# Kernel tuning notes

Measured on AMD Instinct MI355X. Metric: run time of the kernel, lower is better.

## Reference

```python
import jax, jax.numpy as jnp
import numpy as np

NEG_BIG = -9e15  # matches torch's -9000000000000000.0 mask value
ALPHA = 0.2      # LeakyReLU negative slope


def setup_inputs() -> dict:
    key = jax.random.key(0)
    k1, k2, k3 = jax.random.split(key, 3)
    B, N, Fin, Fout = 8, 2048, 64, 64
    h = jax.random.normal(k1, (B, N, Fin), dtype=jnp.float32)
    adj = jax.random.randint(k2, (B, N, N), 0, 2, dtype=jnp.int32)
    kW, ka = jax.random.split(k3)
    # xavier_uniform with gain=1.414
    gW = 1.414 * np.sqrt(6.0 / (Fin + Fout))
    W = jax.random.uniform(kW, (Fin, Fout), minval=-gW, maxval=gW, dtype=jnp.float32)
    ga = 1.414 * np.sqrt(6.0 / (2 * Fout + 1))
    a = jax.random.uniform(ka, (2 * Fout, 1), minval=-ga, maxval=ga, dtype=jnp.float32)
    return {"h": h, "adj": adj, "W": W, "a": a}


def reference(h, adj, W, a):
    # Wh: [B, N, Fout]
    Wh = jnp.einsum("bnf,fo->bno", h, W)
    Fout = W.shape[1]
    a1 = a[:Fout, 0]   # source part of attention vector
    a2 = a[Fout:, 0]   # target part
    # e_ij = leakyrelu(a1.Wh_i + a2.Wh_j) -- rank-1 decomposition of the
    # repeat/cat construction; avoids the [B,N,N,2F] intermediate.
    s = Wh @ a1        # [B, N]
    t = Wh @ a2        # [B, N]
    e = s[:, :, None] + t[:, None, :]            # [B, N, N]
    e = jnp.where(e > 0, e, ALPHA * e)           # LeakyReLU
    e = jnp.where(adj > 0, e, NEG_BIG)           # adjacency mask
    attention = jax.nn.softmax(e, axis=2)
    # dropout omitted: reference is eval-mode (F.dropout is identity when not training)
    h_prime = jnp.einsum("bij,bjo->bio", attention, Wh)
    return jax.nn.elu(h_prime)                   # concat=True branch
```

## Files before the change

kernel.cpp:

```cpp
#include <hip/hip_runtime.h>


#define ALPHA 0.2f

typedef __attribute__((ext_vector_type(8))) short  short8;
typedef __attribute__((ext_vector_type(4))) float  f32x4;

static __device__ __forceinline__ unsigned short f2bf(float f) {
    unsigned u = __builtin_bit_cast(unsigned, f);
    u += 0x7fffu + ((u >> 16) & 1u);
    return (unsigned short)(u >> 16);
}

static __device__ __forceinline__ unsigned pack_bf2(float lo, float hi) {
    unsigned ulo = __builtin_bit_cast(unsigned, lo) + 0x8000u;
    unsigned uhi = __builtin_bit_cast(unsigned, hi) + 0x8000u;
    return __builtin_amdgcn_perm(uhi, ulo, 0x07060302);
}

__global__ __launch_bounds__(256) void k01(
    const float* __restrict__ h, const int* __restrict__ adj,
    const float* __restrict__ W, const float* __restrict__ a,
    uint4* __restrict__ whF, float* __restrict__ sw,
    float* __restrict__ tw, unsigned char* __restrict__ mask)
{
    __shared__ float W_l[64 * 65];
    __shared__ float wa[128];
    __shared__ float tile[4 * 16 * 65];

    const int tid = threadIdx.x;

    if (blockIdx.x >= 256) {
        const int mb = blockIdx.x - 256;
        const int4* a4 = (const int4*)adj;
        #pragma unroll 1
        for (int g0 = 0; g0 < 16; g0 += 4) {
            int4 v0a, v0b, v1a, v1b, v2a, v2b, v3a, v3b;
            const size_t p0 = (size_t)mb * 4096 + (size_t)g0 * 256 + tid;
            v0a = a4[p0 * 2];          v0b = a4[p0 * 2 + 1];
            v1a = a4[(p0 + 256) * 2];  v1b = a4[(p0 + 256) * 2 + 1];
            v2a = a4[(p0 + 512) * 2];  v2b = a4[(p0 + 512) * 2 + 1];
            v3a = a4[(p0 + 768) * 2];  v3b = a4[(p0 + 768) * 2 + 1];
            unsigned b0 = (v0a.x ? 1u:0u)|(v0a.y ? 2u:0u)|(v0a.z ? 4u:0u)|(v0a.w ? 8u:0u)
                        | (v0b.x ?16u:0u)|(v0b.y ?32u:0u)|(v0b.z ?64u:0u)|(v0b.w ?128u:0u);
            unsigned b1 = (v1a.x ? 1u:0u)|(v1a.y ? 2u:0u)|(v1a.z ? 4u:0u)|(v1a.w ? 8u:0u)
                        | (v1b.x ?16u:0u)|(v1b.y ?32u:0u)|(v1b.z ?64u:0u)|(v1b.w ?128u:0u);
            unsigned b2 = (v2a.x ? 1u:0u)|(v2a.y ? 2u:0u)|(v2a.z ? 4u:0u)|(v2a.w ? 8u:0u)
                        | (v2b.x ?16u:0u)|(v2b.y ?32u:0u)|(v2b.z ?64u:0u)|(v2b.w ?128u:0u);
            unsigned b3 = (v3a.x ? 1u:0u)|(v3a.y ? 2u:0u)|(v3a.z ? 4u:0u)|(v3a.w ? 8u:0u)
                        | (v3b.x ?16u:0u)|(v3b.y ?32u:0u)|(v3b.z ?64u:0u)|(v3b.w ?128u:0u);
            mask[p0]       = (unsigned char)b0;
            mask[p0 + 256] = (unsigned char)b1;
            mask[p0 + 512] = (unsigned char)b2;
            mask[p0 + 768] = (unsigned char)b3;
        }
        return;
    }

    const int lane = tid & 63, wv = tid >> 6;
    const int im   = lane & 15, kq = lane >> 4;

    #pragma unroll
    for (int k = 0; k < 16; ++k) {
        int e = tid + 256 * k;
        W_l[(e >> 6) * 65 + (e & 63)] = W[e];
    }
    __syncthreads();

    if (tid < 128) {
        int f = tid & 63;
        const float* ap = a + (tid >> 6) * 64;
        float acc = 0.f;
        #pragma unroll 8
        for (int o = 0; o < 64; ++o) acc += W_l[f * 65 + o] * ap[o];
        wa[tid] = acc;
    }
    __syncthreads();

    short8 bf[4][2];
    #pragma unroll
    for (int nb = 0; nb < 4; ++nb)
        #pragma unroll
        for (int ks = 0; ks < 2; ++ks)
            #pragma unroll
            for (int u = 0; u < 8; ++u)
                bf[nb][ks][u] = (short)f2bf(W_l[(ks * 32 + kq * 8 + u) * 65 + nb * 16 + im]);

    const int row0 = blockIdx.x * 64 + wv * 16;
    const float* hrow = h + (size_t)(row0 + im) * 64;

    float hv[2][8];
    short8 af[2];
    float sp = 0.f, tp = 0.f;
    #pragma unroll
    for (int ks = 0; ks < 2; ++ks) {
        float4 A = *(const float4*)(hrow + ks * 32 + kq * 8);
        float4 Bv = *(const float4*)(hrow + ks * 32 + kq * 8 + 4);
        hv[ks][0] = A.x;  hv[ks][1] = A.y;  hv[ks][2] = A.z;  hv[ks][3] = A.w;
        hv[ks][4] = Bv.x; hv[ks][5] = Bv.y; hv[ks][6] = Bv.z; hv[ks][7] = Bv.w;
        #pragma unroll
        for (int u = 0; u < 8; ++u) {
            int f = ks * 32 + kq * 8 + u;
            sp += hv[ks][u] * wa[f];
            tp += hv[ks][u] * wa[64 + f];
            af[ks][u] = (short)f2bf(hv[ks][u]);
        }
    }
    sp += __shfl_xor(sp, 16, 64); sp += __shfl_xor(sp, 32, 64);
    tp += __shfl_xor(tp, 16, 64); tp += __shfl_xor(tp, 32, 64);
    if (lane < 16) {
        sw[row0 + lane] = sp;
        tw[row0 + lane] = tp;
    }

    f32x4 acc[4] = {{0.f,0.f,0.f,0.f},{0.f,0.f,0.f,0.f},{0.f,0.f,0.f,0.f},{0.f,0.f,0.f,0.f}};
    #pragma unroll
    for (int ks = 0; ks < 2; ++ks)
        #pragma unroll
        for (int nb = 0; nb < 4; ++nb)
            acc[nb] = __builtin_amdgcn_mfma_f32_16x16x32_bf16(af[ks], bf[nb][ks], acc[nb], 0, 0, 0);

    #pragma unroll
    for (int nb = 0; nb < 4; ++nb)
        #pragma unroll
        for (int r = 0; r < 4; ++r)
            tile[wv * 1040 + (kq * 4 + r) * 65 + nb * 16 + im] = acc[nb][r];
    __syncthreads();

    {
        const int blk_row0 = blockIdx.x * 64;
        const int bb2 = blk_row0 >> 11;
        const int c_base = (blk_row0 & 2047) >> 5;
        #pragma unroll
        for (int k = 0; k < 2; ++k) {
            int e = tid + 256 * k;
            int l = e & 63, ot = (e >> 6) & 3, cl_ = e >> 8;
            int o = ot * 16 + (l & 15);
            int jb = cl_ * 32 + (l >> 4) * 8;
            unsigned d0, d1, d2, d3;
            {
                int j0 = jb;
                d0 = pack_bf2(tile[(j0 >> 4) * 1040 + (j0 & 15) * 65 + o],
                              tile[(j0 >> 4) * 1040 + ((j0 & 15) + 1) * 65 + o]);
                j0 = jb + 2;
                d1 = pack_bf2(tile[(j0 >> 4) * 1040 + (j0 & 15) * 65 + o],
                              tile[(j0 >> 4) * 1040 + ((j0 & 15) + 1) * 65 + o]);
                j0 = jb + 4;
                d2 = pack_bf2(tile[(j0 >> 4) * 1040 + (j0 & 15) * 65 + o],
                              tile[(j0 >> 4) * 1040 + ((j0 & 15) + 1) * 65 + o]);
                j0 = jb + 6;
                d3 = pack_bf2(tile[(j0 >> 4) * 1040 + (j0 & 15) * 65 + o],
                              tile[(j0 >> 4) * 1040 + ((j0 & 15) + 1) * 65 + o]);
            }
            uint4 val = {d0, d1, d2, d3};
            whF[(size_t)(((bb2 * 64 + c_base + cl_) * 4 + ot)) * 64 + l] = val;
        }
    }
}

__global__ __launch_bounds__(256, 2) void k2_attn(
    const unsigned* __restrict__ mask, const uint4* __restrict__ whF,
    const float* __restrict__ sw, const float* __restrict__ tw,
    float* __restrict__ out)
{
    __shared__ float eB[2048];
    __shared__ float eD[2048];
    __shared__ float cpart[4 * 1040];
    __shared__ float zp[64];

    const int tid  = threadIdx.x;
    const int lane = tid & 63, wv = tid >> 6;
    const int im   = lane & 15, kq = lane >> 4;
    const int b    = blockIdx.x >> 7;
    const int i0   = (blockIdx.x & 127) << 4;

    {
        const float4* tp4 = (const float4*)(tw + (size_t)b * 2048);
        float4 t0 = tp4[tid], t1 = tp4[tid + 256];
        float4 e0 = {__expf(t0.x), __expf(t0.y), __expf(t0.z), __expf(t0.w)};
        float4 e1 = {__expf(t1.x), __expf(t1.y), __expf(t1.z), __expf(t1.w)};
        float4 f0 = {__expf(ALPHA*t0.x), __expf(ALPHA*t0.y), __expf(ALPHA*t0.z), __expf(ALPHA*t0.w)};
        float4 f1 = {__expf(ALPHA*t1.x), __expf(ALPHA*t1.y), __expf(ALPHA*t1.z), __expf(ALPHA*t1.w)};
        *(float4*)&eB[tid * 4] = e0;  *(float4*)&eB[(tid + 256) * 4] = e1;
        *(float4*)&eD[tid * 4] = f0;  *(float4*)&eD[(tid + 256) * 4] = f1;
    }

    const uint4* mrow4 = (const uint4*)(mask + (size_t)(b * 2048 + i0 + im) * 64 + wv * 16);
    const uint4 mA = mrow4[0], mB = mrow4[1], mC = mrow4[2], mD = mrow4[3];
    const unsigned mm[16] = {mA.x, mA.y, mA.z, mA.w, mB.x, mB.y, mB.z, mB.w,
                             mC.x, mC.y, mC.z, mC.w, mD.x, mD.y, mD.z, mD.w};

    const float sl = sw[b * 2048 + i0 + im];
    const float al = __expf(sl), cl_ = __expf(ALPHA * sl);
    const int j00 = wv * 512 + kq * 8;
    const uint4* wbase = whF + (size_t)((b * 64 + wv * 16) * 4) * 64 + lane;

    __syncthreads();

    f32x4 acc0 = {0.f,0.f,0.f,0.f}, acc1 = {0.f,0.f,0.f,0.f};
    f32x4 acc2 = {0.f,0.f,0.f,0.f}, acc3 = {0.f,0.f,0.f,0.f};
    float zs = 0.f;

    #pragma unroll
    for (int s = 0; s < 16; ++s) {
        const uint4 w0 = wbase[(s * 4 + 0) * 64];
        const uint4 w1 = wbase[(s * 4 + 1) * 64];
        const uint4 w2 = wbase[(s * 4 + 2) * 64];
        const uint4 w3 = wbase[(s * 4 + 3) * 64];

        const float4 bA = *(const float4*)&eB[j00 + s * 32];
        const float4 bBv = *(const float4*)&eB[j00 + s * 32 + 4];
        const float4 dA = *(const float4*)&eD[j00 + s * 32];
        const float4 dBv = *(const float4*)&eD[j00 + s * 32 + 4];
        const unsigned mbyte = (mm[s] >> (kq * 8)) & 0xffu;

        float m0 = al * bA.x, n0 = cl_ * dA.x;
        float m1 = al * bA.y, n1 = cl_ * dA.y;
        float m2 = al * bA.z, n2 = cl_ * dA.z;
        float m3 = al * bA.w, n3 = cl_ * dA.w;
        float m4 = al * bBv.x, n4 = cl_ * dBv.x;
        float m5 = al * bBv.y, n5 = cl_ * dBv.y;
        float m6 = al * bBv.z, n6 = cl_ * dBv.z;
        float m7 = al * bBv.w, n7 = cl_ * dBv.w;

        float p0 = m0 > 1.f ? m0 : n0;  p0 = (mbyte &   1u) ? p0 : 0.f;
        float p1 = m1 > 1.f ? m1 : n1;  p1 = (mbyte &   2u) ? p1 : 0.f;
        float p2 = m2 > 1.f ? m2 : n2;  p2 = (mbyte &   4u) ? p2 : 0.f;
        float p3 = m3 > 1.f ? m3 : n3;  p3 = (mbyte &   8u) ? p3 : 0.f;
        float p4 = m4 > 1.f ? m4 : n4;  p4 = (mbyte &  16u) ? p4 : 0.f;
        float p5 = m5 > 1.f ? m5 : n5;  p5 = (mbyte &  32u) ? p5 : 0.f;
        float p6 = m6 > 1.f ? m6 : n6;  p6 = (mbyte &  64u) ? p6 : 0.f;
        float p7 = m7 > 1.f ? m7 : n7;  p7 = (mbyte & 128u) ? p7 : 0.f;

        zs += ((p0 + p1) + (p2 + p3)) + ((p4 + p5) + (p6 + p7));

        int4 ai;
        ai.x = (int)pack_bf2(p0, p1);
        ai.y = (int)pack_bf2(p2, p3);
        ai.z = (int)pack_bf2(p4, p5);
        ai.w = (int)pack_bf2(p6, p7);
        const short8 af = __builtin_bit_cast(short8, ai);

        acc0 = __builtin_amdgcn_mfma_f32_16x16x32_bf16(af, __builtin_bit_cast(short8, w0), acc0, 0, 0, 0);
        acc1 = __builtin_amdgcn_mfma_f32_16x16x32_bf16(af, __builtin_bit_cast(short8, w1), acc1, 0, 0, 0);
        acc2 = __builtin_amdgcn_mfma_f32_16x16x32_bf16(af, __builtin_bit_cast(short8, w2), acc2, 0, 0, 0);
        acc3 = __builtin_amdgcn_mfma_f32_16x16x32_bf16(af, __builtin_bit_cast(short8, w3), acc3, 0, 0, 0);
    }

    zs += __shfl_xor(zs, 16, 64);
    zs += __shfl_xor(zs, 32, 64);
    if (lane < 16) zp[wv * 16 + lane] = zs;

    #pragma unroll
    for (int r = 0; r < 4; ++r) {
        cpart[wv * 1040 + (kq * 4 + r) * 65 +  0 + im] = acc0[r];
        cpart[wv * 1040 + (kq * 4 + r) * 65 + 16 + im] = acc1[r];
        cpart[wv * 1040 + (kq * 4 + r) * 65 + 32 + im] = acc2[r];
        cpart[wv * 1040 + (kq * 4 + r) * 65 + 48 + im] = acc3[r];
    }
    __syncthreads();

    #pragma unroll
    for (int k = 0; k < 4; ++k) {
        int idx = tid + 256 * k;
        int i = idx >> 6, o = idx & 63;
        float ssum = cpart[0 * 1040 + i * 65 + o] + cpart[1 * 1040 + i * 65 + o]
                   + cpart[2 * 1040 + i * 65 + o] + cpart[3 * 1040 + i * 65 + o];
        float z = zp[i] + zp[16 + i] + zp[32 + i] + zp[48 + i];
        if (z == 0.f) z = 1.f;
        float r = ssum / z;
        out[((size_t)(b * 2048 + i0 + i)) * 64 + o] = r > 0.f ? r : expm1f(r);
    }
}

extern "C" void kernel_launch(void* const* d_in, const int* in_sizes, int n_in,
                              void* d_out, int out_size, void* d_ws, size_t ws_size,
                              hipStream_t stream) {
    const float* h   = (const float*)d_in[0];
    const int*   adj = (const int*)d_in[1];
    const float* W   = (const float*)d_in[2];
    const float* a   = (const float*)d_in[3];
    float* out = (float*)d_out;

    uint4* whF = (uint4*)d_ws;
    float* sw  = (float*)((char*)d_ws + 2097152);
    float* tw  = (float*)((char*)d_ws + 2097152 + 65536);
    unsigned char* mask = (unsigned char*)((char*)d_ws + 2097152 + 131072);

    hipLaunchKernelGGL(k01, dim3(1280), dim3(256), 0, stream, h, adj, W, a, whF, sw, tw, mask);
    hipLaunchKernelGGL(k2_attn, dim3(1024), dim3(256), 0, stream,
                       (const unsigned*)mask, whF, sw, tw, out);
}
```

Measured before the change: 214.8 us.

## Process 32 query rows per block, reuse Wh fragments, compute row sums via MFMA

The attention kernel now handles 32 rows per block instead of 16, so each loaded Wh fragment and each exp table entry feeds two sets of MFMAs and the grid is halved. The softmax denominator moves from VALU adds and shuffles onto an extra MFMA against a ones vector, and the LeakyReLU select becomes fmaxf. The epilogue writes float4 and uses a reciprocal. In exchange, registers and LDS roughly double per block, which may reduce occupancy, and 512 blocks may underfill the GPU. The denominator is also now accumulated from the bf16-rounded weights.

```diff
diff --git a/kernel.cpp b/kernel.cpp
--- a/kernel.cpp
+++ b/kernel.cpp
@@ -165,14 +165,13 @@
 {
     __shared__ float eB[2048];
     __shared__ float eD[2048];
-    __shared__ float cpart[4 * 1040];
-    __shared__ float zp[64];
+    __shared__ float cpart[4 * 2176];
 
     const int tid  = threadIdx.x;
     const int lane = tid & 63, wv = tid >> 6;
     const int im   = lane & 15, kq = lane >> 4;
-    const int b    = blockIdx.x >> 7;
-    const int i0   = (blockIdx.x & 127) << 4;
+    const int b    = blockIdx.x >> 6;
+    const int i0   = (blockIdx.x & 63) << 5;
 
     {
         const float4* tp4 = (const float4*)(tw + (size_t)b * 2048);
@@ -185,21 +184,37 @@
         *(float4*)&eD[tid * 4] = f0;  *(float4*)&eD[(tid + 256) * 4] = f1;
     }
 
-    const uint4* mrow4 = (const uint4*)(mask + (size_t)(b * 2048 + i0 + im) * 64 + wv * 16);
-    const uint4 mA = mrow4[0], mB = mrow4[1], mC = mrow4[2], mD = mrow4[3];
-    const unsigned mm[16] = {mA.x, mA.y, mA.z, mA.w, mB.x, mB.y, mB.z, mB.w,
-                             mC.x, mC.y, mC.z, mC.w, mD.x, mD.y, mD.z, mD.w};
-
-    const float sl = sw[b * 2048 + i0 + im];
-    const float al = __expf(sl), cl_ = __expf(ALPHA * sl);
+    const uint4* mr0 = (const uint4*)(mask + (size_t)(b * 2048 + i0 + im) * 64 + wv * 16);
+    const uint4* mr1 = (const uint4*)(mask + (size_t)(b * 2048 + i0 + 16 + im) * 64 + wv * 16);
+    const uint4 mA0 = mr0[0], mB0 = mr0[1], mC0 = mr0[2], mD0 = mr0[3];
+    const uint4 mA1 = mr1[0], mB1 = mr1[1], mC1 = mr1[2], mD1 = mr1[3];
+    const unsigned mm0[16] = {mA0.x, mA0.y, mA0.z, mA0.w, mB0.x, mB0.y, mB0.z, mB0.w,
+                              mC0.x, mC0.y, mC0.z, mC0.w, mD0.x, mD0.y, mD0.z, mD0.w};
+    const unsigned mm1[16] = {mA1.x, mA1.y, mA1.z, mA1.w, mB1.x, mB1.y, mB1.z, mB1.w,
+                              mC1.x, mC1.y, mC1.z, mC1.w, mD1.x, mD1.y, mD1.z, mD1.w};
+
+    const float sl0 = sw[b * 2048 + i0 + im];
+    const float sl1 = sw[b * 2048 + i0 + 16 + im];
+    const float al0 = __expf(sl0), cl0 = __expf(ALPHA * sl0);
+    const float al1 = __expf(sl1), cl1 = __expf(ALPHA * sl1);
+
     const int j00 = wv * 512 + kq * 8;
     const uint4* wbase = whF + (size_t)((b * 64 + wv * 16) * 4) * 64 + lane;
 
+    short8 onesf;
+    {
+        const short ov = (im == 0) ? (short)0x3F80 : (short)0;
+        #pragma unroll
+        for (int u = 0; u < 8; ++u) onesf[u] = ov;
+    }
+
     __syncthreads();
 
     f32x4 acc0 = {0.f,0.f,0.f,0.f}, acc1 = {0.f,0.f,0.f,0.f};
     f32x4 acc2 = {0.f,0.f,0.f,0.f}, acc3 = {0.f,0.f,0.f,0.f};
-    float zs = 0.f;
+    f32x4 acc4 = {0.f,0.f,0.f,0.f}, acc5 = {0.f,0.f,0.f,0.f};
+    f32x4 acc6 = {0.f,0.f,0.f,0.f}, acc7 = {0.f,0.f,0.f,0.f};
+    f32x4 az0  = {0.f,0.f,0.f,0.f}, az1  = {0.f,0.f,0.f,0.f};
 
     #pragma unroll
     for (int s = 0; s < 16; ++s) {
@@ -208,68 +223,98 @@
         const uint4 w2 = wbase[(s * 4 + 2) * 64];
         const uint4 w3 = wbase[(s * 4 + 3) * 64];
 
-        const float4 bA = *(const float4*)&eB[j00 + s * 32];
+        const float4 bA  = *(const float4*)&eB[j00 + s * 32];
         const float4 bBv = *(const float4*)&eB[j00 + s * 32 + 4];
-        const float4 dA = *(const float4*)&eD[j00 + s * 32];
+        const float4 dA  = *(const float4*)&eD[j00 + s * 32];
         const float4 dBv = *(const float4*)&eD[j00 + s * 32 + 4];
-        const unsigned mbyte = (mm[s] >> (kq * 8)) & 0xffu;
-
-        float m0 = al * bA.x, n0 = cl_ * dA.x;
-        float m1 = al * bA.y, n1 = cl_ * dA.y;
-        float m2 = al * bA.z, n2 = cl_ * dA.z;
-        float m3 = al * bA.w, n3 = cl_ * dA.w;
-        float m4 = al * bBv.x, n4 = cl_ * dBv.x;
-        float m5 = al * bBv.y, n5 = cl_ * dBv.y;
-        float m6 = al * bBv.z, n6 = cl_ * dBv.z;
-        float m7 = al * bBv.w, n7 = cl_ * dBv.w;
-
-        float p0 = m0 > 1.f ? m0 : n0;  p0 = (mbyte &   1u) ? p0 : 0.f;
-        float p1 = m1 > 1.f ? m1 : n1;  p1 = (mbyte &   2u) ? p1 : 0.f;
-        float p2 = m2 > 1.f ? m2 : n2;  p2 = (mbyte &   4u) ? p2 : 0.f;
-        float p3 = m3 > 1.f ? m3 : n3;  p3 = (mbyte &   8u) ? p3 : 0.f;
-        float p4 = m4 > 1.f ? m4 : n4;  p4 = (mbyte &  16u) ? p4 : 0.f;
-        float p5 = m5 > 1.f ? m5 : n5;  p5 = (mbyte &  32u) ? p5 : 0.f;
-        float p6 = m6 > 1.f ? m6 : n6;  p6 = (mbyte &  64u) ? p6 : 0.f;
-        float p7 = m7 > 1.f ? m7 : n7;  p7 = (mbyte & 128u) ? p7 : 0.f;
-
-        zs += ((p0 + p1) + (p2 + p3)) + ((p4 + p5) + (p6 + p7));
-
-        int4 ai;
-        ai.x = (int)pack_bf2(p0, p1);
-        ai.y = (int)pack_bf2(p2, p3);
-        ai.z = (int)pack_bf2(p4, p5);
-        ai.w = (int)pack_bf2(p6, p7);
-        const short8 af = __builtin_bit_cast(short8, ai);
-
-        acc0 = __builtin_amdgcn_mfma_f32_16x16x32_bf16(af, __builtin_bit_cast(short8, w0), acc0, 0, 0, 0);
-        acc1 = __builtin_amdgcn_mfma_f32_16x16x32_bf16(af, __builtin_bit_cast(short8, w1), acc1, 0, 0, 0);
-        acc2 = __builtin_amdgcn_mfma_f32_16x16x32_bf16(af, __builtin_bit_cast(short8, w2), acc2, 0, 0, 0);
-        acc3 = __builtin_amdgcn_mfma_f32_16x16x32_bf16(af, __builtin_bit_cast(short8, w3), acc3, 0, 0, 0);
-    }
-
-    zs += __shfl_xor(zs, 16, 64);
-    zs += __shfl_xor(zs, 32, 64);
-    if (lane < 16) zp[wv * 16 + lane] = zs;
+        const unsigned mb0 = (mm0[s] >> (kq * 8)) & 0xffu;
+        const unsigned mb1 = (mm1[s] >> (kq * 8)) & 0xffu;
+
+        float p0 = fmaxf(al0 * bA.x,  cl0 * dA.x);   p0 = (mb0 &   1u) ? p0 : 0.f;
+        float p1 = fmaxf(al0 * bA.y,  cl0 * dA.y);   p1 = (mb0 &   2u) ? p1 : 0.f;
+        float p2 = fmaxf(al0 * bA.z,  cl0 * dA.z);   p2 = (mb0 &   4u) ? p2 : 0.f;
+        float p3 = fmaxf(al0 * bA.w,  cl0 * dA.w);   p3 = (mb0 &   8u) ? p3 : 0.f;
+        float p4 = fmaxf(al0 * bBv.x, cl0 * dBv.x);  p4 = (mb0 &  16u) ? p4 : 0.f;
+        float p5 = fmaxf(al0 * bBv.y, cl0 * dBv.y);  p5 = (mb0 &  32u) ? p5 : 0.f;
+        float p6 = fmaxf(al0 * bBv.z, cl0 * dBv.z);  p6 = (mb0 &  64u) ? p6 : 0.f;
+        float p7 = fmaxf(al0 * bBv.w, cl0 * dBv.w);  p7 = (mb0 & 128u) ? p7 : 0.f;
+
+        int4 ai0;
+        ai0.x = (int)pack_bf2(p0, p1);
+        ai0.y = (int)pack_bf2(p2, p3);
+        ai0.z = (int)pack_bf2(p4, p5);
+        ai0.w = (int)pack_bf2(p6, p7);
+        const short8 af0 = __builtin_bit_cast(short8, ai0);
+
+        float q0 = fmaxf(al1 * bA.x,  cl1 * dA.x);   q0 = (mb1 &   1u) ? q0 : 0.f;
+        float q1 = fmaxf(al1 * bA.y,  cl1 * dA.y);   q1 = (mb1 &   2u) ? q1 : 0.f;
+        float q2 = fmaxf(al1 * bA.z,  cl1 * dA.z);   q2 = (mb1 &   4u) ? q2 : 0.f;
+        float q3 = fmaxf(al1 * bA.w,  cl1 * dA.w);   q3 = (mb1 &   8u) ? q3 : 0.f;
+        float q4 = fmaxf(al1 * bBv.x, cl1 * dBv.x);  q4 = (mb1 &  16u) ? q4 : 0.f;
+        float q5 = fmaxf(al1 * bBv.y, cl1 * dBv.y);  q5 = (mb1 &  32u) ? q5 : 0.f;
+        float q6 = fmaxf(al1 * bBv.z, cl1 * dBv.z);  q6 = (mb1 &  64u) ? q6 : 0.f;
+        float q7 = fmaxf(al1 * bBv.w, cl1 * dBv.w);  q7 = (mb1 & 128u) ? q7 : 0.f;
+
+        int4 ai1;
+        ai1.x = (int)pack_bf2(q0, q1);
+        ai1.y = (int)pack_bf2(q2, q3);
+        ai1.z = (int)pack_bf2(q4, q5);
+        ai1.w = (int)pack_bf2(q6, q7);
+        const short8 af1 = __builtin_bit_cast(short8, ai1);
+
+        acc0 = __builtin_amdgcn_mfma_f32_16x16x32_bf16(af0, __builtin_bit_cast(short8, w0), acc0, 0, 0, 0);
+        acc1 = __builtin_amdgcn_mfma_f32_16x16x32_bf16(af0, __builtin_bit_cast(short8, w1), acc1, 0, 0, 0);
+        acc2 = __builtin_amdgcn_mfma_f32_16x16x32_bf16(af0, __builtin_bit_cast(short8, w2), acc2, 0, 0, 0);
+        acc3 = __builtin_amdgcn_mfma_f32_16x16x32_bf16(af0, __builtin_bit_cast(short8, w3), acc3, 0, 0, 0);
+        az0  = __builtin_amdgcn_mfma_f32_16x16x32_bf16(af0, onesf, az0, 0, 0, 0);
+
+        acc4 = __builtin_amdgcn_mfma_f32_16x16x32_bf16(af1, __builtin_bit_cast(short8, w0), acc4, 0, 0, 0);
+        acc5 = __builtin_amdgcn_mfma_f32_16x16x32_bf16(af1, __builtin_bit_cast(short8, w1), acc5, 0, 0, 0);
+        acc6 = __builtin_amdgcn_mfma_f32_16x16x32_bf16(af1, __builtin_bit_cast(short8, w2), acc6, 0, 0, 0);
+        acc7 = __builtin_amdgcn_mfma_f32_16x16x32_bf16(af1, __builtin_bit_cast(short8, w3), acc7, 0, 0, 0);
+        az1  = __builtin_amdgcn_mfma_f32_16x16x32_bf16(af1, onesf, az1, 0, 0, 0);
+    }
 
     #pragma unroll
     for (int r = 0; r < 4; ++r) {
-        cpart[wv * 1040 + (kq * 4 + r) * 65 +  0 + im] = acc0[r];
-        cpart[wv * 1040 + (kq * 4 + r) * 65 + 16 + im] = acc1[r];
-        cpart[wv * 1040 + (kq * 4 + r) * 65 + 32 + im] = acc2[r];
-        cpart[wv * 1040 + (kq * 4 + r) * 65 + 48 + im] = acc3[r];
-    }
-    __syncthreads();
-
-    #pragma unroll
-    for (int k = 0; k < 4; ++k) {
-        int idx = tid + 256 * k;
-        int i = idx >> 6, o = idx & 63;
-        float ssum = cpart[0 * 1040 + i * 65 + o] + cpart[1 * 1040 + i * 65 + o]
-                   + cpart[2 * 1040 + i * 65 + o] + cpart[3 * 1040 + i * 65 + o];
-        float z = zp[i] + zp[16 + i] + zp[32 + i] + zp[48 + i];
+        const int row = kq * 4 + r;
+        float* cp0 = &cpart[wv * 2176 + row * 68];
+        cp0[ 0 + im] = acc0[r];
+        cp0[16 + im] = acc1[r];
+        cp0[32 + im] = acc2[r];
+        cp0[48 + im] = acc3[r];
+        float* cp1 = &cpart[wv * 2176 + (16 + row) * 68];
+        cp1[ 0 + im] = acc4[r];
+        cp1[16 + im] = acc5[r];
+        cp1[32 + im] = acc6[r];
+        cp1[48 + im] = acc7[r];
+        if (im == 0) { cp0[64] = az0[r]; cp1[64] = az1[r]; }
+    }
+    __syncthreads();
+
+    #pragma unroll
+    for (int k = 0; k < 2; ++k) {
+        const int idx4 = tid + 256 * k;
+        const int i  = idx4 >> 4;
+        const int oc = (idx4 & 15) << 2;
+        const float4 s0 = *(const float4*)&cpart[0 * 2176 + i * 68 + oc];
+        const float4 s1 = *(const float4*)&cpart[1 * 2176 + i * 68 + oc];
+        const float4 s2 = *(const float4*)&cpart[2 * 2176 + i * 68 + oc];
+        const float4 s3 = *(const float4*)&cpart[3 * 2176 + i * 68 + oc];
+        float z = cpart[0 * 2176 + i * 68 + 64] + cpart[1 * 2176 + i * 68 + 64]
+                + cpart[2 * 2176 + i * 68 + 64] + cpart[3 * 2176 + i * 68 + 64];
         if (z == 0.f) z = 1.f;
-        float r = ssum / z;
-        out[((size_t)(b * 2048 + i0 + i)) * 64 + o] = r > 0.f ? r : expm1f(r);
+        const float inv = 1.f / z;
+        float4 rv;
+        rv.x = ((s0.x + s1.x) + (s2.x + s3.x)) * inv;
+        rv.y = ((s0.y + s1.y) + (s2.y + s3.y)) * inv;
+        rv.z = ((s0.z + s1.z) + (s2.z + s3.z)) * inv;
+        rv.w = ((s0.w + s1.w) + (s2.w + s3.w)) * inv;
+        rv.x = rv.x > 0.f ? rv.x : expm1f(rv.x);
+        rv.y = rv.y > 0.f ? rv.y : expm1f(rv.y);
+        rv.z = rv.z > 0.f ? rv.z : expm1f(rv.z);
+        rv.w = rv.w > 0.f ? rv.w : expm1f(rv.w);
+        *(float4*)(out + ((size_t)(b * 2048 + i0 + i)) * 64 + oc) = rv;
     }
 }
 
@@ -288,6 +333,6 @@
     unsigned char* mask = (unsigned char*)((char*)d_ws + 2097152 + 131072);
 
     hipLaunchKernelGGL(k01, dim3(1280), dim3(256), 0, stream, h, adj, W, a, whF, sw, tw, mask);
-    hipLaunchKernelGGL(k2_attn, dim3(1024), dim3(256), 0, stream,
+    hipLaunchKernelGGL(k2_attn, dim3(512), dim3(256), 0, stream,
                        (const unsigned*)mask, whF, sw, tw, out);
 }
```

Measured after the change: 212.8 us. About the same (-0.9%).
